# Kernel optimization log

Hardware: AMD Instinct MI355X
Metric: run time of the kernel (lower is better)

Reference implementation:

```python
import jax, jax.numpy as jnp
import numpy as np
import math

NX = 240
XL = 6.0
A_ORB = 2
V0 = -20.0
S_INT = 0.5
ITERMAX = 500
FFAC = 0.4


def _wfho(n, x):
    # harmonic-oscillator eigenfunction (numpy, setup only)
    nfac = math.factorial(n)
    norm = (2.0 ** n * nfac) ** (-0.5) / math.pi ** 0.25
    if n == 0:
        Hn = np.ones_like(x)
    elif n == 1:
        Hn = 2.0 * x
    else:
        hm2 = np.ones_like(x)
        hm1 = 2.0 * x
        for m in range(2, n + 1):
            hmx = 2.0 * x * hm1 - 2.0 * (m - 1) * hm2
            hm2, hm1 = hm1, hmx
        Hn = hmx
    return norm * np.exp(-x ** 2 / 2.0) * Hn


def setup_inputs() -> dict:
    delx = 2.0 * XL / NX
    xx = delx * (np.arange(NX) - NX / 2.0)
    delp = 2.0 * math.pi / (2.0 * XL)
    pp = delp * (np.arange(NX) - NX / 2.0)
    # cder2[i,j] = sum_k exp(1j*(xj-xi)*pp_k) * pp_k^2 ; only real part is used
    D = xx[None, :] - xx[:, None]                      # [Nx, Nx], xj - xi
    cder2_re = np.cos(D[:, :, None] * pp[None, None, :]) @ (pp ** 2)
    der2 = -cder2_re * delx * delp / (2.0 * math.pi)
    kin = -der2 / 2.0
    pfac = 1.0 / abs(kin.max())
    U_HO = xx ** 2 / 2.0
    x1, x2 = np.meshgrid(xx, xx, indexing='ij')
    Vint = V0 * (2.0 * math.pi) ** (-0.5) / S_INT * np.exp(-(x1 - x2) ** 2 / (2.0 * S_INT ** 2))
    wfy0 = np.stack([_wfho(n, xx) for n in range(A_ORB)], axis=1)  # [Nx, Nmax]
    return {
        'wfy0': jnp.asarray(wfy0, jnp.float32),
        'kin_mat': jnp.asarray(kin, jnp.float32),
        'Vint': jnp.asarray(Vint, jnp.float32),
        'U_HO': jnp.asarray(U_HO, jnp.float32),
        'delx': jnp.float32(delx),
        'pfac': jnp.float32(pfac),
        'itermax': ITERMAX,
    }


def reference(wfy0, kin_mat, Vint, U_HO, delx, pfac, itermax):
    Nmax = wfy0.shape[1]
    delx = jnp.asarray(delx, jnp.float32).reshape(())
    pfac = jnp.asarray(pfac, jnp.float32).reshape(())

    def step(wfy, _):
        # densities from current orbitals
        hf_den = jnp.sum(wfy ** 2, axis=1)            # [Nx]
        hf_den_mat = wfy @ wfy.T                      # [Nx, Nx]
        Udir = delx * (Vint @ hf_den)
        Umf_mat = -delx * Vint * hf_den_mat
        Umf_mat = Umf_mat + jnp.diag(Udir + U_HO)     # add to diagonal
        H = kin_mat + Umf_mat

        updated = []
        spe = []
        ekin = jnp.float32(0.0)
        epot = jnp.float32(0.0)
        for ieig in range(Nmax):                      # Nmax=2, unrolled
            wf0 = wfy[:, ieig]
            wff = H @ wf0
            spe.append((wf0 @ wff) * delx)
            wfb = wf0 - wff * pfac
            norm = jnp.sum(wfb ** 2) * delx
            wff = wfb / jnp.sqrt(norm)
            for jeig in range(ieig):                  # Gram-Schmidt vs already-updated orbitals
                wff = wff - updated[jeig] * (updated[jeig] @ wff) * delx
            norm = jnp.sum(wff ** 2) * delx
            wff = wff / norm                          # faithful: divide by norm (not sqrt)
            new = FFAC * wff + (1.0 - FFAC) * wf0
            updated.append(new)
            ekin = ekin + (new @ (kin_mat @ new)) * delx
            epot = epot + (new @ (Umf_mat @ new)) * delx
        wfy_new = jnp.stack(updated, axis=1)

        esum0hf = spe[0]
        for s_ in spe[1:]:
            esum0hf = esum0hf + s_
        eho = jnp.sum(hf_den * U_HO) * delx / 2.0
        enerhfp = (esum0hf + ekin) / 2.0 + eho
        epot0hf = epot - 2.0 * eho
        enerhf = esum0hf - epot0hf / 2.0
        out = jnp.stack([enerhf, enerhfp, ekin, eho, epot0hf, esum0hf])
        return wfy_new, out

    _, outs = jax.lax.scan(step, wfy0, None, length=int(itermax))
    return outs[-1]  # (enerhf, enerhfp, ekin0hf, eho, epot0hf, esum0hf)
```

## Files before the change

### kernel.cpp

```cpp
#include <hip/hip_runtime.h>


#define NXX  240
#define NPAD 256
#define NTH  512
#define JCH  60
#define NBLK 15
#define NQW  16

template <int CTRL>
__device__ __forceinline__ float dppAddStep(float x) {
  int s = __builtin_amdgcn_update_dpp(0, __float_as_int(x), CTRL, 0xF, 0xF, false);
  return x + __int_as_float(s);
}
__device__ __forceinline__ float waveSumDpp(float x) {
  x = dppAddStep<0xB1>(x);
  x = dppAddStep<0x4E>(x);
  x = dppAddStep<0x141>(x);
  x = dppAddStep<0x140>(x);
  x = dppAddStep<0x142>(x);
  x = dppAddStep<0x143>(x);
  return __int_as_float(__builtin_amdgcn_readlane(__float_as_int(x), 63));
}

struct __align__(16) Smem {
  float cK[512];
  float cV[512];
  float uho[NPAD];
  float wfb[2][2][NPAD];
  float p00[NPAD];
  float p01[NPAD];
  float p11[NPAD];
  float part[4][6][NPAD];
};

__global__ void __launch_bounds__(NTH, 2)
hf_kernel(const float* __restrict__ wfy0,
          const float* __restrict__ kin,
          const float* __restrict__ vnt,
          const float* __restrict__ uho_g,
          const float* __restrict__ delx_p,
          const float* __restrict__ pfac_p,
          const int*   __restrict__ iter_p,
          float* __restrict__ out)
{
  __shared__ Smem sm;
  const int t  = (int)threadIdx.x;
  const int wv = t >> 6;
  const int l  = t & 63;
  const int i0 = 4 * l;
  const bool isK = (wv < 4);
  const int g  = isK ? wv : wv - 4;
  const int jg = g * JCH;
  const float delx = delx_p[0];
  const float pfac = pfac_p[0];
  const int itermax = iter_p[0];

  for (int a = t; a < 512; a += NTH) {
    int d = a - 256;
    float vk = 0.f, vv = 0.f;
    if (d >= 0 && d < NXX)      { vk = kin[(size_t)d * NXX]; vv = vnt[(size_t)d * NXX]; }
    else if (d < 0 && -d < NXX) { vk = kin[-d];              vv = vnt[-d]; }
    sm.cK[a] = vk; sm.cV[a] = vv;
  }
  if (t < NPAD) {
    float u  = (t < NXX) ? uho_g[t]        : 0.f;
    float a0 = (t < NXX) ? wfy0[2 * t]     : 0.f;
    float a1 = (t < NXX) ? wfy0[2 * t + 1] : 0.f;
    sm.uho[t] = u;
    sm.wfb[0][0][t] = a0; sm.wfb[0][1][t] = a1;
    sm.wfb[1][0][t] = 0.f; sm.wfb[1][1][t] = 0.f;
    sm.p00[t] = a0 * a0; sm.p01[t] = a0 * a1; sm.p11[t] = a1 * a1;
  }
  __syncthreads();

  const int qb = l - 15 * g + 49;
  const float* tab = isK ? sm.cK : sm.cV;
  float4 cw[NQW];
#pragma unroll
  for (int m = 0; m < NQW; ++m)
    cw[m] = *(const float4*)&tab[4 * (qb + m)];

  int cur = 0;
  for (int it = 0; it < itermax; ++it) {
    const bool last = (it == itermax - 1);
    const float* wf0 = sm.wfb[cur][0];
    const float* wf1 = sm.wfb[cur][1];
    float* nw0 = sm.wfb[cur ^ 1][0];
    float* nw1 = sm.wfb[cur ^ 1][1];

    if (isK) {
      float aK0[4] = {0,0,0,0}, aK1[4] = {0,0,0,0};
#pragma unroll
      for (int b = 0; b < NBLK; ++b) {
        const int j0 = jg + 4 * b;
        const float4 x0 = *(const float4*)&wf0[j0];
        const float4 x1 = *(const float4*)&wf1[j0];
        const float4 kh = cw[15 - b], kl = cw[14 - b];
        const float ck[8] = {kl.x, kl.y, kl.z, kl.w, kh.x, kh.y, kh.z, kh.w};
        const float xs0[4] = {x0.x, x0.y, x0.z, x0.w};
        const float xs1[4] = {x1.x, x1.y, x1.z, x1.w};
#pragma unroll
        for (int s = 0; s < 4; ++s) {
#pragma unroll
          for (int r = 0; r < 4; ++r) {
            const int c = 4 + r - s;
            aK0[r] = fmaf(xs0[s], ck[c], aK0[r]);
            aK1[r] = fmaf(xs1[s], ck[c], aK1[r]);
          }
        }
      }
      *(float4*)&sm.part[g][0][i0] = make_float4(aK0[0], aK0[1], aK0[2], aK0[3]);
      *(float4*)&sm.part[g][1][i0] = make_float4(aK1[0], aK1[1], aK1[2], aK1[3]);
    } else {
      float aV0[4] = {0,0,0,0}, aV1[4] = {0,0,0,0}, aV2[4] = {0,0,0,0};
#pragma unroll
      for (int b = 0; b < NBLK; ++b) {
        const int j0 = jg + 4 * b;
        const float4 y0 = *(const float4*)&sm.p00[j0];
        const float4 y1 = *(const float4*)&sm.p01[j0];
        const float4 y2 = *(const float4*)&sm.p11[j0];
        const float4 vh = cw[15 - b], vl = cw[14 - b];
        const float cv[8] = {vl.x, vl.y, vl.z, vl.w, vh.x, vh.y, vh.z, vh.w};
        const float ys0[4] = {y0.x, y0.y, y0.z, y0.w};
        const float ys1[4] = {y1.x, y1.y, y1.z, y1.w};
        const float ys2[4] = {y2.x, y2.y, y2.z, y2.w};
#pragma unroll
        for (int s = 0; s < 4; ++s) {
#pragma unroll
          for (int r = 0; r < 4; ++r) {
            const int c = 4 + r - s;
            aV0[r] = fmaf(ys0[s], cv[c], aV0[r]);
            aV1[r] = fmaf(ys1[s], cv[c], aV1[r]);
            aV2[r] = fmaf(ys2[s], cv[c], aV2[r]);
          }
        }
      }
      *(float4*)&sm.part[g][2][i0] = make_float4(aV0[0], aV0[1], aV0[2], aV0[3]);
      *(float4*)&sm.part[g][3][i0] = make_float4(aV1[0], aV1[1], aV1[2], aV1[3]);
      *(float4*)&sm.part[g][4][i0] = make_float4(aV2[0], aV2[1], aV2[2], aV2[3]);
    }
    __syncthreads();

    float w0[4], w1[4], Ut[4], wff0[4], wff1[4], new0[4], new1[4];
    float spe0 = 0.f, spe1 = 0.f, eho = 0.f;

    if (wv == 0) {
      const bool valid = (l < 60);
      float k0[4]  = {0,0,0,0}, k1[4]  = {0,0,0,0};
      float v00[4] = {0,0,0,0}, v01[4] = {0,0,0,0}, v11[4] = {0,0,0,0};
#pragma unroll
      for (int gg = 0; gg < 4; ++gg) {
        const float4 A0 = *(const float4*)&sm.part[gg][0][i0];
        const float4 A1 = *(const float4*)&sm.part[gg][1][i0];
        const float4 A2 = *(const float4*)&sm.part[gg][2][i0];
        const float4 A3 = *(const float4*)&sm.part[gg][3][i0];
        const float4 A4 = *(const float4*)&sm.part[gg][4][i0];
        k0[0]  += A0.x; k0[1]  += A0.y; k0[2]  += A0.z; k0[3]  += A0.w;
        k1[0]  += A1.x; k1[1]  += A1.y; k1[2]  += A1.z; k1[3]  += A1.w;
        v00[0] += A2.x; v00[1] += A2.y; v00[2] += A2.z; v00[3] += A2.w;
        v01[0] += A3.x; v01[1] += A3.y; v01[2] += A3.z; v01[3] += A3.w;
        v11[0] += A4.x; v11[1] += A4.y; v11[2] += A4.z; v11[3] += A4.w;
      }
      const float4 w0q = *(const float4*)&wf0[i0];
      const float4 w1q = *(const float4*)&wf1[i0];
      const float4 uq  = *(const float4*)&sm.uho[i0];
      w0[0] = w0q.x; w0[1] = w0q.y; w0[2] = w0q.z; w0[3] = w0q.w;
      w1[0] = w1q.x; w1[1] = w1q.y; w1[2] = w1q.z; w1[3] = w1q.w;
      const float uh[4] = {uq.x, uq.y, uq.z, uq.w};

      float wb0[4], wb1[4];
      float s0 = 0.f, s1 = 0.f;
#pragma unroll
      for (int r = 0; r < 4; ++r) {
        Ut[r]   = delx * (v00[r] + v11[r]) + uh[r];
        wff0[r] = k0[r] - delx * (w0[r] * v00[r] + w1[r] * v01[r]) + Ut[r] * w0[r];
        wff1[r] = k1[r] - delx * (w0[r] * v01[r] + w1[r] * v11[r]) + Ut[r] * w1[r];
        wb0[r]  = w0[r] - pfac * wff0[r];
        wb1[r]  = w1[r] - pfac * wff1[r];
        if (!valid) { wb0[r] = 0.f; wb1[r] = 0.f; }
        s0 += wb0[r] * wb0[r];
        s1 += wb1[r] * wb1[r];
      }
      s0 = waveSumDpp(s0);
      s1 = waveSumDpp(s1);
      const float inv0 = 1.f / sqrtf(s0 * delx);
      const float inv1 = 1.f / sqrtf(s1 * delx);
      float wfA[4], wfBp[4], sA = 0.f;
#pragma unroll
      for (int r = 0; r < 4; ++r) {
        wfA[r]  = wb0[r] * inv0;
        wfBp[r] = wb1[r] * inv1;
        sA += wfA[r] * wfA[r];
      }
      sA = waveSumDpp(sA);
      const float invA = 1.f / (sA * delx);
      float sd = 0.f;
#pragma unroll
      for (int r = 0; r < 4; ++r) {
        new0[r] = 0.4f * (wfA[r] * invA) + 0.6f * w0[r];
        sd += new0[r] * wfBp[r];
      }
      sd = waveSumDpp(sd);
      const float dB = sd * delx;
      float wfB2[4], sB = 0.f;
#pragma unroll
      for (int r = 0; r < 4; ++r) {
        wfB2[r] = wfBp[r] - new0[r] * dB;
        sB += wfB2[r] * wfB2[r];
      }
      sB = waveSumDpp(sB);
      const float invB = 1.f / (sB * delx);
#pragma unroll
      for (int r = 0; r < 4; ++r)
        new1[r] = 0.4f * (wfB2[r] * invB) + 0.6f * w1[r];

      *(float4*)&nw0[i0] = make_float4(new0[0], new0[1], new0[2], new0[3]);
      *(float4*)&nw1[i0] = make_float4(new1[0], new1[1], new1[2], new1[3]);
      *(float4*)&sm.p00[i0] =
          make_float4(new0[0]*new0[0], new0[1]*new0[1], new0[2]*new0[2], new0[3]*new0[3]);
      *(float4*)&sm.p01[i0] =
          make_float4(new0[0]*new1[0], new0[1]*new1[1], new0[2]*new1[2], new0[3]*new1[3]);
      *(float4*)&sm.p11[i0] =
          make_float4(new1[0]*new1[0], new1[1]*new1[1], new1[2]*new1[2], new1[3]*new1[3]);

      if (last) {
        float sp0 = 0.f, sp1 = 0.f, se = 0.f;
#pragma unroll
        for (int r = 0; r < 4; ++r) {
          sp0 += w0[r] * wff0[r];
          sp1 += w1[r] * wff1[r];
          se  += (w0[r] * w0[r] + w1[r] * w1[r]) * uh[r];
        }
        sp0 = waveSumDpp(sp0);
        sp1 = waveSumDpp(sp1);
        se  = waveSumDpp(se);
        spe0 = sp0 * delx; spe1 = sp1 * delx; eho = se * delx * 0.5f;
      }
    }
    __syncthreads();

    if (last) {
      if (isK) {
        float bA0[4] = {0,0,0,0}, bA1[4] = {0,0,0,0};
#pragma unroll
        for (int b = 0; b < NBLK; ++b) {
          const int j0 = jg + 4 * b;
          const float4 n0q = *(const float4*)&nw0[j0];
          const float4 n1q = *(const float4*)&nw1[j0];
          const float4 kh = cw[15 - b], kl = cw[14 - b];
          const float ck[8] = {kl.x, kl.y, kl.z, kl.w, kh.x, kh.y, kh.z, kh.w};
          const float xn0[4] = {n0q.x, n0q.y, n0q.z, n0q.w};
          const float xn1[4] = {n1q.x, n1q.y, n1q.z, n1q.w};
#pragma unroll
          for (int s = 0; s < 4; ++s) {
#pragma unroll
            for (int r = 0; r < 4; ++r) {
              const int c = 4 + r - s;
              bA0[r] = fmaf(xn0[s], ck[c], bA0[r]);
              bA1[r] = fmaf(xn1[s], ck[c], bA1[r]);
            }
          }
        }
        *(float4*)&sm.part[g][0][i0] = make_float4(bA0[0], bA0[1], bA0[2], bA0[3]);
        *(float4*)&sm.part[g][1][i0] = make_float4(bA1[0], bA1[1], bA1[2], bA1[3]);
      } else {
        float bV[4][4] = {};
#pragma unroll
        for (int b = 0; b < NBLK; ++b) {
          const int j0 = jg + 4 * b;
          const float4 o0q = *(const float4*)&wf0[j0];
          const float4 o1q = *(const float4*)&wf1[j0];
          const float4 n0q = *(const float4*)&nw0[j0];
          const float4 n1q = *(const float4*)&nw1[j0];
          const float4 vh = cw[15 - b], vl = cw[14 - b];
          const float cv[8] = {vl.x, vl.y, vl.z, vl.w, vh.x, vh.y, vh.z, vh.w};
          const float xo0[4] = {o0q.x, o0q.y, o0q.z, o0q.w};
          const float xo1[4] = {o1q.x, o1q.y, o1q.z, o1q.w};
          const float xn0[4] = {n0q.x, n0q.y, n0q.z, n0q.w};
          const float xn1[4] = {n1q.x, n1q.y, n1q.z, n1q.w};
#pragma unroll
          for (int s = 0; s < 4; ++s) {
            const float pr00 = xo0[s] * xn0[s];
            const float pr10 = xo1[s] * xn0[s];
            const float pr01 = xo0[s] * xn1[s];
            const float pr11 = xo1[s] * xn1[s];
#pragma unroll
            for (int r = 0; r < 4; ++r) {
              const int c = 4 + r - s;
              bV[0][r] = fmaf(pr00, cv[c], bV[0][r]);
              bV[1][r] = fmaf(pr10, cv[c], bV[1][r]);
              bV[2][r] = fmaf(pr01, cv[c], bV[2][r]);
              bV[3][r] = fmaf(pr11, cv[c], bV[3][r]);
            }
          }
        }
#pragma unroll
        for (int c2 = 0; c2 < 4; ++c2)
          *(float4*)&sm.part[g][2 + c2][i0] =
              make_float4(bV[c2][0], bV[c2][1], bV[c2][2], bV[c2][3]);
      }
      __syncthreads();

      if (wv == 0) {
        float rd[6][4] = {};
#pragma unroll
        for (int gg = 0; gg < 4; ++gg) {
#pragma unroll
          for (int c = 0; c < 6; ++c) {
            const float4 A = *(const float4*)&sm.part[gg][c][i0];
            rd[c][0] += A.x; rd[c][1] += A.y; rd[c][2] += A.z; rd[c][3] += A.w;
          }
        }
        float re = 0.f, rp = 0.f;
#pragma unroll
        for (int r = 0; r < 4; ++r) {
          const float um0 = -delx * (w0[r] * rd[2][r] + w1[r] * rd[3][r]) + Ut[r] * new0[r];
          const float um1 = -delx * (w0[r] * rd[4][r] + w1[r] * rd[5][r]) + Ut[r] * new1[r];
          re += new0[r] * rd[0][r] + new1[r] * rd[1][r];
          rp += new0[r] * um0 + new1[r] * um1;
        }
        re = waveSumDpp(re);
        rp = waveSumDpp(rp);
        const float ekin = re * delx, epot = rp * delx;
        if (l == 0) {
          const float esum    = spe0 + spe1;
          const float enerhfp = 0.5f * (esum + ekin) + eho;
          const float epot0hf = epot - 2.f * eho;
          const float enerhf  = esum - 0.5f * epot0hf;
          out[0] = enerhf; out[1] = enerhfp; out[2] = ekin;
          out[3] = eho;    out[4] = epot0hf; out[5] = esum;
        }
      }
    }
    cur ^= 1;
  }
}

extern "C" void kernel_launch(void* const* d_in, const int* in_sizes, int n_in,
                              void* d_out, int out_size, void* d_ws, size_t ws_size,
                              hipStream_t stream) {
  const float* wfy0 = (const float*)d_in[0];
  const float* kin  = (const float*)d_in[1];
  const float* vnt  = (const float*)d_in[2];
  const float* uho  = (const float*)d_in[3];
  const float* delx = (const float*)d_in[4];
  const float* pfac = (const float*)d_in[5];
  const int*   itm  = (const int*)d_in[6];
  hipLaunchKernelGGL(hf_kernel, dim3(1), dim3(NTH), 0, stream,
                     wfy0, kin, vnt, uho, delx, pfac, itm, (float*)d_out);
}
```

Baseline: 1.321 ms.

## Collapse serial wave reductions into one batched reduction via closed-form norms

The orbital update chain of four dependent wave reductions (norm, norm of normalized, overlap, norm after Gram-Schmidt) is replaced by one batched DPP reduction of six dot products. The later norms and overlaps are then derived algebraically from those sums. The DPP helper is generalized to reduce several values interleaved, which also batches the energy reductions. This shortens the serial reduction latency on each iteration's critical path. The price is a different floating-point rounding path, since norms are computed by expansion rather than directly, which risks cancellation in sB.

```diff
diff --git a/kernel.cpp b/kernel.cpp
--- a/kernel.cpp
+++ b/kernel.cpp
@@ -8,19 +8,25 @@
 #define NBLK 15
 #define NQW  16
 
-template <int CTRL>
-__device__ __forceinline__ float dppAddStep(float x) {
-  int s = __builtin_amdgcn_update_dpp(0, __float_as_int(x), CTRL, 0xF, 0xF, false);
-  return x + __int_as_float(s);
+template <int CTRL, int N>
+__device__ __forceinline__ void dppStepN(float (&v)[N]) {
+#pragma unroll
+  for (int k = 0; k < N; ++k) {
+    int s = __builtin_amdgcn_update_dpp(0, __float_as_int(v[k]), CTRL, 0xF, 0xF, false);
+    v[k] += __int_as_float(s);
+  }
 }
-__device__ __forceinline__ float waveSumDpp(float x) {
-  x = dppAddStep<0xB1>(x);
-  x = dppAddStep<0x4E>(x);
-  x = dppAddStep<0x141>(x);
-  x = dppAddStep<0x140>(x);
-  x = dppAddStep<0x142>(x);
-  x = dppAddStep<0x143>(x);
-  return __int_as_float(__builtin_amdgcn_readlane(__float_as_int(x), 63));
+template <int N>
+__device__ __forceinline__ void waveSumDppN(float (&v)[N]) {
+  dppStepN<0xB1>(v);
+  dppStepN<0x4E>(v);
+  dppStepN<0x141>(v);
+  dppStepN<0x140>(v);
+  dppStepN<0x142>(v);
+  dppStepN<0x143>(v);
+#pragma unroll
+  for (int k = 0; k < N; ++k)
+    v[k] = __int_as_float(__builtin_amdgcn_readlane(__float_as_int(v[k]), 63));
 }
 
 struct __align__(16) Smem {
@@ -170,7 +176,7 @@
       const float uh[4] = {uq.x, uq.y, uq.z, uq.w};
 
       float wb0[4], wb1[4];
-      float s0 = 0.f, s1 = 0.f;
+      float red[6] = {0, 0, 0, 0, 0, 0};
 #pragma unroll
       for (int r = 0; r < 4; ++r) {
         Ut[r]   = delx * (v00[r] + v11[r]) + uh[r];
@@ -179,42 +185,29 @@
         wb0[r]  = w0[r] - pfac * wff0[r];
         wb1[r]  = w1[r] - pfac * wff1[r];
         if (!valid) { wb0[r] = 0.f; wb1[r] = 0.f; }
-        s0 += wb0[r] * wb0[r];
-        s1 += wb1[r] * wb1[r];
-      }
-      s0 = waveSumDpp(s0);
-      s1 = waveSumDpp(s1);
-      const float inv0 = 1.f / sqrtf(s0 * delx);
-      const float inv1 = 1.f / sqrtf(s1 * delx);
-      float wfA[4], wfBp[4], sA = 0.f;
+        red[0] += wb0[r] * wb0[r];
+        red[1] += wb1[r] * wb1[r];
+        red[2] += wb0[r] * wb1[r];
+        red[3] += w0[r]  * wb1[r];
+        red[4] += wb0[r] * w0[r];
+        red[5] += w0[r]  * w0[r];
+      }
+      waveSumDppN<6>(red);
+      const float rdelx = 1.f / delx;
+      const float inv0 = 1.f / sqrtf(red[0] * delx);
+      const float inv1 = 1.f / sqrtf(red[1] * delx);
+      const float dB = delx * inv1 * (0.4f * red[2] * inv0 + 0.6f * red[3]);
+      const float e0 = 0.16f * rdelx + 0.48f * red[4] * inv0 + 0.36f * red[5];
+      const float sB = rdelx - dB * dB * (2.f * rdelx - e0);
+      const float invB = 1.f / (sB * delx);
 #pragma unroll
       for (int r = 0; r < 4; ++r) {
-        wfA[r]  = wb0[r] * inv0;
-        wfBp[r] = wb1[r] * inv1;
-        sA += wfA[r] * wfA[r];
-      }
-      sA = waveSumDpp(sA);
-      const float invA = 1.f / (sA * delx);
-      float sd = 0.f;
-#pragma unroll
-      for (int r = 0; r < 4; ++r) {
-        new0[r] = 0.4f * (wfA[r] * invA) + 0.6f * w0[r];
-        sd += new0[r] * wfBp[r];
-      }
-      sd = waveSumDpp(sd);
-      const float dB = sd * delx;
-      float wfB2[4], sB = 0.f;
-#pragma unroll
-      for (int r = 0; r < 4; ++r) {
-        wfB2[r] = wfBp[r] - new0[r] * dB;
-        sB += wfB2[r] * wfB2[r];
-      }
-      sB = waveSumDpp(sB);
-      const float invB = 1.f / (sB * delx);
-#pragma unroll
-      for (int r = 0; r < 4; ++r)
-        new1[r] = 0.4f * (wfB2[r] * invB) + 0.6f * w1[r];
-
+        const float wfA  = wb0[r] * inv0;
+        const float wfBp = wb1[r] * inv1;
+        new0[r] = 0.4f * wfA + 0.6f * w0[r];
+        const float wfB2 = wfBp - new0[r] * dB;
+        new1[r] = 0.4f * wfB2 * invB + 0.6f * w1[r];
+      }
       *(float4*)&nw0[i0] = make_float4(new0[0], new0[1], new0[2], new0[3]);
       *(float4*)&nw1[i0] = make_float4(new1[0], new1[1], new1[2], new1[3]);
       *(float4*)&sm.p00[i0] =
@@ -225,17 +218,15 @@
           make_float4(new1[0]*new1[0], new1[1]*new1[1], new1[2]*new1[2], new1[3]*new1[3]);
 
       if (last) {
-        float sp0 = 0.f, sp1 = 0.f, se = 0.f;
+        float er[3] = {0, 0, 0};
 #pragma unroll
         for (int r = 0; r < 4; ++r) {
-          sp0 += w0[r] * wff0[r];
-          sp1 += w1[r] * wff1[r];
-          se  += (w0[r] * w0[r] + w1[r] * w1[r]) * uh[r];
-        }
-        sp0 = waveSumDpp(sp0);
-        sp1 = waveSumDpp(sp1);
-        se  = waveSumDpp(se);
-        spe0 = sp0 * delx; spe1 = sp1 * delx; eho = se * delx * 0.5f;
+          er[0] += w0[r] * wff0[r];
+          er[1] += w1[r] * wff1[r];
+          er[2] += (w0[r] * w0[r] + w1[r] * w1[r]) * uh[r];
+        }
+        waveSumDppN<3>(er);
+        spe0 = er[0] * delx; spe1 = er[1] * delx; eho = er[2] * delx * 0.5f;
       }
     }
     __syncthreads();
@@ -312,17 +303,16 @@
             rd[c][0] += A.x; rd[c][1] += A.y; rd[c][2] += A.z; rd[c][3] += A.w;
           }
         }
-        float re = 0.f, rp = 0.f;
+        float er[2] = {0, 0};
 #pragma unroll
         for (int r = 0; r < 4; ++r) {
           const float um0 = -delx * (w0[r] * rd[2][r] + w1[r] * rd[3][r]) + Ut[r] * new0[r];
           const float um1 = -delx * (w0[r] * rd[4][r] + w1[r] * rd[5][r]) + Ut[r] * new1[r];
-          re += new0[r] * rd[0][r] + new1[r] * rd[1][r];
-          rp += new0[r] * um0 + new1[r] * um1;
-        }
-        re = waveSumDpp(re);
-        rp = waveSumDpp(rp);
-        const float ekin = re * delx, epot = rp * delx;
+          er[0] += new0[r] * rd[0][r] + new1[r] * rd[1][r];
+          er[1] += new0[r] * um0 + new1[r] * um1;
+        }
+        waveSumDppN<2>(er);
+        const float ekin = er[0] * delx, epot = er[1] * delx;
         if (l == 0) {
           const float esum    = spe0 + spe1;
           const float enerhfp = 0.5f * (esum + ekin) + eho;
```

Result: faster. 1.282 ms (-3.0%).
